# Kernel tuning notes

Hardware: AMD Instinct MI355X
Metric: run time of the kernel (lower is better)

The kernel has to match this reference:

```python
import jax, jax.numpy as jnp
import numpy as np

T, B, L, CTX, H = 512, 512, 16, 64, 128
STATE_DIM, SHOT, PID, DATA = 32, 12, 35, 23


def setup_inputs() -> dict:
    key = jax.random.key(0)
    ks = jax.random.split(key, 64)
    k = iter(ks)
    def rn(shape, s=0.1):
        return (jax.random.normal(next(k), shape) * s).astype(jnp.float32)
    xs = jax.random.normal(next(k), (T, B, DATA), jnp.float32)
    xs = xs.at[:, :, 12].set(jax.random.randint(next(k), (T, B), 0, SHOT).astype(jnp.float32))
    xs = xs.at[:, :, 17].set(jax.random.randint(next(k), (T, B), 0, PID).astype(jnp.float32))
    xs = xs.at[:, :, 20].set(jax.random.randint(next(k), (T, B), 0, SHOT).astype(jnp.float32))
    return dict(
        total_xs=jnp.zeros((1,), jnp.float32),
        xs=xs,
        ts=jnp.linspace(0.0, 2.0, T).astype(jnp.float32),
        noise_std=jnp.asarray(0.1, jnp.float32),
        z0_noise=jax.random.normal(next(k), (B, L), jnp.float32),
        bm_noise=jax.random.normal(next(k), (T - 1, B, L), jnp.float32),
        shot_emb=rn((SHOT, 8)), player_emb=rn((PID, 8)),
        gru_wih=rn((3 * H, STATE_DIM)), gru_whh=rn((3 * H, H)),
        gru_bih=rn((3 * H,)), gru_bhh=rn((3 * H,)),
        enc_w=rn((CTX, H)), enc_b=rn((CTX,)),
        qz0_w=rn((2 * L, CTX)), qz0_b=rn((2 * L,)),
        f_w1=rn((H, L + CTX)), f_b1=rn((H,)), f_w2=rn((H, H)), f_b2=rn((H,)),
        f_w3=rn((L, H)), f_b3=rn((L,)),
        h_w1=rn((H, L)), h_b1=rn((H,)), h_w2=rn((H, H)), h_b2=rn((H,)),
        h_w3=rn((L, H)), h_b3=rn((L,)),
        g_w1=rn((L, H)), g_b1=rn((L, H)), g_w2=rn((L, H)), g_b2=rn((L,)),
        proj_w=rn((STATE_DIM, L)), proj_b=rn((STATE_DIM,)),
        pz0_mean=jnp.zeros((1, L), jnp.float32), pz0_logstd=jnp.zeros((1, L), jnp.float32),
        act_w=rn((128, L)), act_b=rn((128,)),
        act_land_w=rn((2, 128)), act_shot_w=rn((SHOT, 128)), act_move_w=rn((2, 128)),
    )


def _forward(xs, noise_std, shot_emb, player_emb, gru_wih, gru_whh, gru_bih, gru_bhh,
             enc_w, enc_b, qz0_w, qz0_b,
             f_w1, f_b1, f_w2, f_b2, f_w3, f_b3,
             h_w1, h_b1, h_w2, h_b2, h_w3, h_b3,
             g_w1, g_b1, g_w2, g_b2,
             proj_w, proj_b, pz0_mean, pz0_logstd,
             act_w, act_b, act_land_w, act_shot_w, act_move_w,
             ts, z0_noise, bm_noise):
    # --- SDE_embed_and_transform: replace shot/player id cols with embeddings ---
    state = xs[:, :, :18]
    shot_ids = state[:, :, 12].astype(jnp.int32)
    pid_ids = state[:, :, 17].astype(jnp.int32)
    state_t = jnp.concatenate([state[:, :, :12], shot_emb[shot_ids],
                               state[:, :, 13:17], player_emb[pid_ids]], axis=-1)  # (T,B,32)
    xs_t = jnp.concatenate([state_t, xs[:, :, 18:]], axis=-1)  # (T,B,37)
    # --- Encoder: GRU over time-reversed states, linear head, flip back ---
    def gru_step(h, xt):
        gi = xt @ gru_wih.T + gru_bih
        gh = h @ gru_whh.T + gru_bhh
        ir, iz, inn = jnp.split(gi, 3, axis=-1)
        hr, hz, hn = jnp.split(gh, 3, axis=-1)
        r = jax.nn.sigmoid(ir + hr)
        zg = jax.nn.sigmoid(iz + hz)
        n = jnp.tanh(inn + r * hn)
        hnew = (1.0 - zg) * n + zg * h
        return hnew, hnew
    h0 = jnp.zeros((xs.shape[1], gru_whh.shape[1]), xs.dtype)
    _, hs = jax.lax.scan(gru_step, h0, state_t[::-1])
    ctx = (hs @ enc_w.T + enc_b)[::-1]  # (T,B,CTX)
    # --- posterior z0 ---
    qm, qls = jnp.split(ctx[0] @ qz0_w.T + qz0_b, 2, axis=1)
    z0 = qm + jnp.exp(qls) * z0_noise
    # --- Euler-Maruyama with logqp; searchsorted(right) -> ctx[min(i+1,T-1)] = ctx[i+1] ---
    dts = ts[1:] - ts[:-1]  # (T-1,)
    dW = jnp.sqrt(dts)[:, None, None] * bm_noise
    ctx_steps = ctx[1:]
    def mlp3(x, w1, b1, w2, b2, w3, b3):
        h1 = jax.nn.softplus(x @ w1.T + b1)
        h2 = jax.nn.softplus(h1 @ w2.T + b2)
        return h2 @ w3.T + b3
    def g_diag(y):  # (B,L): per-latent-dim scalar nets, batched over L
        hg = jax.nn.softplus(y[:, :, None] * g_w1[None] + g_b1[None])  # (B,L,H)
        return jax.nn.sigmoid(jnp.einsum('blh,lh->bl', hg, g_w2) + g_b2)
    def sde_step(z, inp):
        c, dw, dt = inp
        f_val = mlp3(jnp.concatenate([z, c], axis=1), f_w1, f_b1, f_w2, f_b2, f_w3, f_b3)
        h_val = mlp3(z, h_w1, h_b1, h_w2, h_b2, h_w3, h_b3)
        g_val = g_diag(z)
        u = (f_val - h_val) / g_val
        logr = 0.5 * jnp.sum(u * u, axis=1) * dt
        z_new = z + f_val * dt + g_val * dw
        return z_new, (z_new, logr)
    _, (z_tail, log_ratio) = jax.lax.scan(sde_step, z0, (ctx_steps, dW, dts))
    zs = jnp.concatenate([z0[None], z_tail], axis=0)  # (T,B,L)
    _xs = zs @ proj_w.T + proj_b  # (T,B,32)
    # --- action model losses ---
    a = jax.nn.relu(zs @ act_w.T + act_b)
    land = (a @ act_land_w.T).reshape(-1, 2)
    shot_logits = (a @ act_shot_w.T).reshape(-1, act_shot_w.shape[0])
    move = (a @ act_move_w.T).reshape(-1, 2)
    true_actions = xs_t[:, :, -5:]
    true_land = true_actions[:, :, :2].reshape(-1, 2)
    true_move = true_actions[:, :, 3:].reshape(-1, 2)
    true_shot = true_actions[:, :, 2].astype(jnp.int32).reshape(-1)
    land_loss = jnp.mean((land - true_land) ** 2)
    move_loss = jnp.mean((move - true_move) ** 2)
    logp = jax.nn.log_softmax(shot_logits, axis=-1)
    picked = jnp.take_along_axis(logp, true_shot[:, None], axis=1)[:, 0]
    mask = (true_shot != 0).astype(logp.dtype)  # CrossEntropy ignore_index=0
    shot_loss = -jnp.sum(picked * mask) / jnp.maximum(jnp.sum(mask), 1.0)
    # --- reconstruction log-likelihood ---
    xs_state = xs_t[:, :, :STATE_DIM]
    LOG2PI = 1.8378770664093453
    log_pxs = jnp.mean(jnp.sum(
        -0.5 * ((xs_state - _xs) / noise_std) ** 2 - jnp.log(noise_std) - 0.5 * LOG2PI,
        axis=(0, 2)))
    # --- KL(q(z0) || p(z0)) ---
    var_q = jnp.exp(2.0 * qls)
    var_p = jnp.exp(2.0 * pz0_logstd)
    kl = pz0_logstd - qls + (var_q + (qm - pz0_mean) ** 2) / (2.0 * var_p) - 0.5
    logqp0 = jnp.mean(jnp.sum(kl, axis=1))
    logqp_path = jnp.mean(jnp.sum(log_ratio, axis=0))
    return log_pxs, logqp0 + logqp_path + land_loss + shot_loss + move_loss


def reference(total_xs, xs, ts, noise_std, z0_noise, bm_noise, shot_emb, player_emb,
              gru_wih, gru_whh, gru_bih, gru_bhh, enc_w, enc_b, qz0_w, qz0_b,
              f_w1, f_b1, f_w2, f_b2, f_w3, f_b3, h_w1, h_b1, h_w2, h_b2, h_w3, h_b3,
              g_w1, g_b1, g_w2, g_b2, proj_w, proj_b, pz0_mean, pz0_logstd,
              act_w, act_b, act_land_w, act_shot_w, act_move_w):
    return _forward(xs, noise_std, shot_emb, player_emb, gru_wih, gru_whh, gru_bih, gru_bhh,
                    enc_w, enc_b, qz0_w, qz0_b,
                    f_w1, f_b1, f_w2, f_b2, f_w3, f_b3,
                    h_w1, h_b1, h_w2, h_b2, h_w3, h_b3,
                    g_w1, g_b1, g_w2, g_b2,
                    proj_w, proj_b, pz0_mean, pz0_logstd,
                    act_w, act_b, act_land_w, act_shot_w, act_move_w,
                    ts, z0_noise, bm_noise)
```

## Files before the change

### kernel.cpp

```cpp
#include <hip/hip_runtime.h>
#include <cstdint>

typedef _Float16 f16;
typedef _Float16 f16x2 __attribute__((ext_vector_type(2)));

#define T_STEPS 512
#define B_SZ 512
#define LOG2PI 1.8378770664093453f

__device__ __forceinline__ void barrier_lds() {
  asm volatile("s_waitcnt lgkmcnt(0)" ::: "memory");
  __builtin_amdgcn_s_barrier();
  asm volatile("" ::: "memory");
}

__device__ __forceinline__ uint32_t packh2(float a, float b) {
  f16x2 v; v[0] = (f16)a; v[1] = (f16)b;
  return __builtin_bit_cast(uint32_t, v);
}

__device__ __forceinline__ float fdot2(uint32_t a, uint32_t b, float c) {
#if defined(__AMDGCN__) && __has_builtin(__builtin_amdgcn_fdot2)
  return __builtin_amdgcn_fdot2(__builtin_bit_cast(f16x2, a),
                                __builtin_bit_cast(f16x2, b), c, false);
#else
  f16x2 x = __builtin_bit_cast(f16x2, a), y = __builtin_bit_cast(f16x2, b);
  return c + (float)x[0] * (float)y[0] + (float)x[1] * (float)y[1];
#endif
}

#define DOT4(acc, w0, w1, w2, w3, v)                                     \
  do {                                                                   \
    acc = fdot2((w0), (v).x, acc); acc = fdot2((w1), (v).y, acc);        \
    acc = fdot2((w2), (v).z, acc); acc = fdot2((w3), (v).w, acc);        \
  } while (0)

__device__ __forceinline__ float sigmoidf_(float x) {
  return 1.0f / (1.0f + __expf(-x));
}
__device__ __forceinline__ float tanhf_(float x) {
  float ax = fabsf(x);
  float t = __expf(-2.0f * ax);
  float r = (1.0f - t) / (1.0f + t);
  return copysignf(r, x);
}
__device__ __forceinline__ float softplusf_(float x) {
  return fmaxf(x, 0.0f) + __logf(1.0f + __expf(-fabsf(x)));
}

__global__ __launch_bounds__(256) void k_embed(
    const float* __restrict__ xs, const float* __restrict__ shot_emb,
    const float* __restrict__ player_emb, f16* __restrict__ state_t,
    float* __restrict__ accums) {
  if (blockIdx.x == 0 && threadIdx.x < 16) accums[threadIdx.x] = 0.0f;
  size_t idx = (size_t)blockIdx.x * 256 + threadIdx.x;
  const float* xp = xs + idx * 23;
  f16* op = state_t + idx * 32;
  int sid = (int)xp[12];
  int pid = (int)xp[17];
#pragma unroll
  for (int i = 0; i < 12; ++i) op[i] = (f16)xp[i];
  const float* se = shot_emb + sid * 8;
#pragma unroll
  for (int i = 0; i < 8; ++i) op[12 + i] = (f16)se[i];
#pragma unroll
  for (int i = 0; i < 4; ++i) op[20 + i] = (f16)xp[13 + i];
  const float* pe = player_emb + pid * 8;
#pragma unroll
  for (int i = 0; i < 8; ++i) op[24 + i] = (f16)pe[i];
}

__global__ __launch_bounds__(256) void k_gtab(
    const float* __restrict__ gw1, const float* __restrict__ gb1,
    const float* __restrict__ gw2, const float* __restrict__ gb2,
    float* __restrict__ g_tab) {
  int gid = blockIdx.x * 256 + threadIdx.x;
  int l = gid >> 16, yi = gid & 0xffff;
  f16 hy = __builtin_bit_cast(f16, (unsigned short)yi);
  float y = (float)hy;
  const float* w1 = gw1 + l * 128;
  const float* b1 = gb1 + l * 128;
  const float* w2 = gw2 + l * 128;
  float a0 = 0.f, a1 = 0.f;
#pragma unroll 8
  for (int h = 0; h < 128; h += 2) {
    a0 = fmaf(softplusf_(fmaf(y, w1[h], b1[h])), w2[h], a0);
    a1 = fmaf(softplusf_(fmaf(y, w1[h + 1], b1[h + 1])), w2[h + 1], a1);
  }
  g_tab[gid] = sigmoidf_(a0 + a1 + gb2[l]);
}

__global__ __launch_bounds__(512) void k_gru(
    const f16* __restrict__ state_t, const float* __restrict__ wih,
    const float* __restrict__ whh, const float* __restrict__ bih,
    const float* __restrict__ bhh, const float* __restrict__ enc_w,
    const float* __restrict__ enc_b, const float* __restrict__ qz0_w,
    const float* __restrict__ qz0_b, const float* __restrict__ z0_noise,
    const float* __restrict__ pz0_mean, const float* __restrict__ pz0_logstd,
    f16* __restrict__ ctx, float* __restrict__ z0_out,
    float* __restrict__ accums) {
  __shared__ uint32_t s_x[2][16];
  __shared__ uint32_t s_h[2][64];
  __shared__ float s_gates[2 * 128 * 4];
  __shared__ float s_encp[2 * 64 * 2];
  __shared__ float s_ctx0[2][64];
  __shared__ float s_q[2][32];

  const int tid = threadIdx.x;
  const int bbase = blockIdx.x * 2;
  const uint32_t* stu = (const uint32_t*)state_t;

  uint32_t wA[64];
  uint32_t wB[16];
  float bias0 = 0.f, bias1 = 0.f, encbr = 0.f;

  if (tid < 256) {
    int g = tid >> 7, du = tid & 127;
    const float* whr = whh + (size_t)(g * 128 + du) * 128;
#pragma unroll
    for (int i = 0; i < 64; ++i) wA[i] = packh2(whr[2 * i], whr[2 * i + 1]);
    const float* wxr = wih + (size_t)(g * 128 + du) * 32;
#pragma unroll
    for (int i = 0; i < 16; ++i) wB[i] = packh2(wxr[2 * i], wxr[2 * i + 1]);
    bias0 = bih[g * 128 + du] + bhh[g * 128 + du];
  } else if (tid < 384) {
    int du = tid - 256;
    const float* whr = whh + (size_t)(256 + du) * 128;
#pragma unroll
    for (int i = 0; i < 64; ++i) wA[i] = packh2(whr[2 * i], whr[2 * i + 1]);
    const float* wxr = wih + (size_t)(256 + du) * 32;
#pragma unroll
    for (int i = 0; i < 16; ++i) wB[i] = packh2(wxr[2 * i], wxr[2 * i + 1]);
    bias0 = bih[256 + du];
    bias1 = bhh[256 + du];
  } else {
    int e = tid - 384, c = e & 63, ks = e >> 6;
    const float* wer = enc_w + (size_t)c * 128 + ks * 64;
#pragma unroll
    for (int i = 0; i < 32; ++i) wA[i] = packh2(wer[2 * i], wer[2 * i + 1]);
    encbr = enc_b[c];
  }

  if (tid < 128) s_h[tid >> 6][tid & 63] = 0u;
  if (tid < 32) {
    int b = tid >> 4, i = tid & 15;
    s_x[b][i] = stu[((size_t)(T_STEPS - 1) * B_SZ + bbase + b) * 16 + i];
  }
  float h_old = 0.0f;
  __syncthreads();

  for (int t = T_STEPS - 1; t >= 0; --t) {
    uint4 xpref = make_uint4(0, 0, 0, 0);
    if (tid < 256) {
      int g = tid >> 7, du = tid & 127;
#pragma unroll
      for (int b = 0; b < 2; ++b) {
        float a = bias0;
        const uint4* xq = (const uint4*)&s_x[b][0];
#pragma unroll
        for (int j = 0; j < 4; ++j) {
          uint4 v = xq[j];
          DOT4(a, wB[4 * j], wB[4 * j + 1], wB[4 * j + 2], wB[4 * j + 3], v);
        }
        const uint4* hq = (const uint4*)&s_h[b][0];
#pragma unroll
        for (int j = 0; j < 16; ++j) {
          uint4 v = hq[j];
          DOT4(a, wA[4 * j], wA[4 * j + 1], wA[4 * j + 2], wA[4 * j + 3], v);
        }
        s_gates[(b * 128 + du) * 4 + g] = a;
      }
    } else if (tid < 384) {
      int du = tid - 256;
#pragma unroll
      for (int b = 0; b < 2; ++b) {
        float aI = bias0, aH = bias1;
        const uint4* xq = (const uint4*)&s_x[b][0];
#pragma unroll
        for (int j = 0; j < 4; ++j) {
          uint4 v = xq[j];
          DOT4(aI, wB[4 * j], wB[4 * j + 1], wB[4 * j + 2], wB[4 * j + 3], v);
        }
        const uint4* hq = (const uint4*)&s_h[b][0];
#pragma unroll
        for (int j = 0; j < 16; ++j) {
          uint4 v = hq[j];
          DOT4(aH, wA[4 * j], wA[4 * j + 1], wA[4 * j + 2], wA[4 * j + 3], v);
        }
        s_gates[(b * 128 + du) * 4 + 2] = aI;
        s_gates[(b * 128 + du) * 4 + 3] = aH;
      }
    } else {
      int e = tid - 384, ks = e >> 6, cc = e & 63;
      (void)cc;
      if (t < T_STEPS - 1) {
#pragma unroll
        for (int b = 0; b < 2; ++b) {
          float a = 0.f;
          const uint4* hq = (const uint4*)&s_h[b][ks * 32];
#pragma unroll
          for (int j = 0; j < 8; ++j) {
            uint4 v = hq[j];
            DOT4(a, wA[4 * j], wA[4 * j + 1], wA[4 * j + 2], wA[4 * j + 3], v);
          }
          s_encp[(b * 64 + cc) * 2 + ks] = a;
        }
      }
      if (e < 8 && t > 0) {
        int b = e & 1, q = e >> 1;
        xpref = *(const uint4*)(stu +
                                ((size_t)(t - 1) * B_SZ + bbase + b) * 16 + q * 4);
      }
    }
    barrier_lds();
    if (tid < 256) {
      int b = tid >> 7, du = tid & 127;
      const float4 gt = *(const float4*)&s_gates[(b * 128 + du) * 4];
      float r = sigmoidf_(gt.x), zg = sigmoidf_(gt.y);
      float n = tanhf_(gt.z + r * gt.w);
      float hnew = (1.0f - zg) * n + zg * h_old;
      h_old = hnew;
      ((f16*)&s_h[b][0])[du] = (f16)hnew;
    } else if (tid >= 384) {
      int e = tid - 384, cc = e & 63, b = e >> 6;
      if (t < T_STEPS - 1) {
        float2 p = *(const float2*)&s_encp[(b * 64 + cc) * 2];
        ctx[((size_t)(t + 1) * B_SZ + bbase + b) * 64 + cc] =
            (f16)(p.x + p.y + encbr);
      }
      if (e < 8 && t > 0) {
        int b2 = e & 1, q = e >> 1;
        *(uint4*)&s_x[b2][q * 4] = xpref;
      }
    }
    barrier_lds();
  }

  if (tid >= 384) {
    int e = tid - 384, ks = e >> 6, cc = e & 63;
#pragma unroll
    for (int b = 0; b < 2; ++b) {
      float a = 0.f;
      const uint4* hq = (const uint4*)&s_h[b][ks * 32];
#pragma unroll
      for (int j = 0; j < 8; ++j) {
        uint4 v = hq[j];
        DOT4(a, wA[4 * j], wA[4 * j + 1], wA[4 * j + 2], wA[4 * j + 3], v);
      }
      s_encp[(b * 64 + cc) * 2 + ks] = a;
    }
  }
  __syncthreads();
  if (tid >= 384) {
    int e = tid - 384, cc = e & 63, b = e >> 6;
    float2 p = *(const float2*)&s_encp[(b * 64 + cc) * 2];
    float val = p.x + p.y + encbr;
    ctx[((size_t)bbase + b) * 64 + cc] = (f16)val;
    s_ctx0[b][cc] = val;
  }
  __syncthreads();
  if (tid < 64) {
    int b = tid >> 5, o = tid & 31;
    float acc = qz0_b[o];
#pragma unroll 8
    for (int k = 0; k < 64; ++k) acc += qz0_w[o * 64 + k] * s_ctx0[b][k];
    s_q[b][o] = acc;
  }
  __syncthreads();
  if (tid < 32) {
    int b = tid >> 4, l = tid & 15;
    int bg = bbase + b;
    float qm = s_q[b][l], qls = s_q[b][16 + l];
    float z0v = qm + __expf(qls) * z0_noise[bg * 16 + l];
    z0_out[bg * 16 + l] = z0v;
    float pm = pz0_mean[l], pls = pz0_logstd[l];
    float var_q = __expf(2.0f * qls);
    float var_p = __expf(2.0f * pls);
    float dm = qm - pm;
    float kl = pls - qls + (var_q + dm * dm) / (2.0f * var_p) - 0.5f;
    atomicAdd(&accums[5], kl);
  }
}

__global__ __launch_bounds__(256, 2) void k_sde(
    const f16* __restrict__ ctx, const float* __restrict__ z0_in,
    const float* __restrict__ ts, const float* __restrict__ bm_noise,
    const float* __restrict__ fw1, const float* __restrict__ fb1,
    const float* __restrict__ fw2, const float* __restrict__ fb2,
    const float* __restrict__ fw3, const float* __restrict__ fb3,
    const float* __restrict__ hw1, const float* __restrict__ hb1,
    const float* __restrict__ hw2, const float* __restrict__ hb2,
    const float* __restrict__ hw3, const float* __restrict__ hb3,
    const float* __restrict__ g_tab,
    f16* __restrict__ zs, float* __restrict__ accums) {
  __shared__ uint32_t s_x2[40];
  __shared__ uint32_t s_h1[2][64];
  __shared__ uint32_t s_h2[2][64];
  __shared__ float s_dts[T_STEPS];

  const int tid = threadIdx.x;
  const int bg = blockIdx.x;
  const uint4* ctx4 = (const uint4*)ctx;

  const int r1 = tid >> 1, hh = tid & 1;
  const int mlp2 = tid >> 7, u2 = tid & 127;
  const int l3 = (tid >> 3) & 15;
  const int mlp3 = (tid >> 2) & 1;
  const int kq = tid & 3;
  const bool p3act = (tid < 128);
  const bool zlane = p3act && ((tid & 7) == 0);
  const bool stg = (tid >= 128 && tid < 136);

  uint32_t uw1f[20], uw1h[4], wP2[64], wP3[16];
  float bf1r, bh1r, bias2r, fb3r = 0.f, hb3r = 0.f;
  {
    const float* w = fw1 + (size_t)r1 * 80 + hh * 40;
#pragma unroll
    for (int i = 0; i < 20; ++i) uw1f[i] = packh2(w[2 * i], w[2 * i + 1]);
    bf1r = fb1[r1];
  }
  {
    const float* w = hw1 + (size_t)r1 * 16 + hh * 8;
#pragma unroll
    for (int i = 0; i < 4; ++i) uw1h[i] = packh2(w[2 * i], w[2 * i + 1]);
    bh1r = hb1[r1];
  }
  {
    const float* w = (mlp2 ? hw2 : fw2) + (size_t)u2 * 128;
#pragma unroll
    for (int i = 0; i < 64; ++i) wP2[i] = packh2(w[2 * i], w[2 * i + 1]);
    bias2r = (mlp2 ? hb2 : fb2)[u2];
  }
  if (p3act) {
    const float* w = (mlp3 ? hw3 : fw3) + (size_t)l3 * 128 + kq * 32;
#pragma unroll
    for (int i = 0; i < 16; ++i) wP3[i] = packh2(w[2 * i], w[2 * i + 1]);
    fb3r = fb3[l3];
    hb3r = hb3[l3];
  }
  for (int i = tid; i < T_STEPS - 1; i += 256) s_dts[i] = ts[i + 1] - ts[i];

  float zreg = 0.f, bmc = 0.f, path_acc = 0.f;
  uint4 cpref = make_uint4(0, 0, 0, 0);
  if (zlane) {
    zreg = z0_in[bg * 16 + l3];
    ((f16*)&s_x2[0])[l3] = (f16)zreg;
    zs[(size_t)bg * 16 + l3] = (f16)zreg;
    bmc = bm_noise[(size_t)bg * 16 + l3];
  }
  if (stg) {
    int q = tid - 128;
    uint4 v = ctx4[((size_t)1 * B_SZ + bg) * 8 + q];
    *(uint4*)&s_x2[8 + q * 4] = v;
  }
  __syncthreads();

  for (int t = 0; t < T_STEPS - 1; ++t) {
    float bmn = 0.f, gvp = 0.f;
    if (zlane) {
      unsigned short zb = __builtin_bit_cast(unsigned short, (f16)zreg);
      gvp = g_tab[l3 * 65536 + (int)zb];
      if (t < T_STEPS - 2)
        bmn = bm_noise[((size_t)(t + 1) * B_SZ + bg) * 16 + l3];
    }
    if (stg && t <= T_STEPS - 3)
      cpref = ctx4[((size_t)(t + 2) * B_SZ + bg) * 8 + (tid - 128)];

    {
      const uint4* xq = (const uint4*)&s_x2[0];
      const int base = hh * 5;
      float a0 = 0.f, a1 = 0.f;
      {
        uint4 v0 = xq[base + 0], v1 = xq[base + 1];
        DOT4(a0, uw1f[0], uw1f[1], uw1f[2], uw1f[3], v0);
        DOT4(a1, uw1f[4], uw1f[5], uw1f[6], uw1f[7], v1);
        uint4 v2 = xq[base + 2], v3 = xq[base + 3];
        DOT4(a0, uw1f[8], uw1f[9], uw1f[10], uw1f[11], v2);
        DOT4(a1, uw1f[12], uw1f[13], uw1f[14], uw1f[15], v3);
        uint4 v4 = xq[base + 4];
        DOT4(a0, uw1f[16], uw1f[17], uw1f[18], uw1f[19], v4);
      }
      float af = a0 + a1;
      uint4 vz = xq[hh];
      float ah = 0.f;
      DOT4(ah, uw1h[0], uw1h[1], uw1h[2], uw1h[3], vz);
      float ff = af + __shfl_xor(af, 1);
      float fh = ah + __shfl_xor(ah, 1);
      if (hh == 0)
        ((f16*)&s_h1[0][0])[r1] = (f16)softplusf_(ff + bf1r);
      else
        ((f16*)&s_h1[1][0])[r1] = (f16)softplusf_(fh + bh1r);
    }
    barrier_lds();
    {
      const uint4* hq = (const uint4*)&s_h1[mlp2][0];
      float a0 = 0.f, a1 = 0.f;
#pragma unroll
      for (int j = 0; j < 16; j += 2) {
        uint4 v0 = hq[j], v1 = hq[j + 1];
        DOT4(a0, wP2[4 * j], wP2[4 * j + 1], wP2[4 * j + 2], wP2[4 * j + 3], v0);
        DOT4(a1, wP2[4 * j + 4], wP2[4 * j + 5], wP2[4 * j + 6], wP2[4 * j + 7], v1);
      }
      ((f16*)&s_h2[mlp2][0])[u2] = (f16)softplusf_(a0 + a1 + bias2r);
    }
    barrier_lds();
    if (p3act) {
      const uint4* hq = (const uint4*)&s_h2[mlp3][kq * 16];
      float a0 = 0.f, a1 = 0.f;
#pragma unroll
      for (int j = 0; j < 4; j += 2) {
        uint4 v0 = hq[j], v1 = hq[j + 1];
        DOT4(a0, wP3[4 * j], wP3[4 * j + 1], wP3[4 * j + 2], wP3[4 * j + 3], v0);
        DOT4(a1, wP3[4 * j + 4], wP3[4 * j + 5], wP3[4 * j + 6], wP3[4 * j + 7], v1);
      }
      float a = a0 + a1;
      float s1 = a + __shfl_xor(a, 1);
      float s2 = s1 + __shfl_xor(s1, 2);
      float other = __shfl_xor(s2, 4);
      if ((tid & 7) == 0) {
        float fv = s2 + fb3r;
        float hv = other + hb3r;
        float gv = gvp;
        float dt = s_dts[t];
        float u_ = (fv - hv) / gv;
        float ls = u_ * u_;
        ls += __shfl_xor(ls, 8);
        ls += __shfl_xor(ls, 16);
        ls += __shfl_xor(ls, 32);
        if ((tid & 63) == 0) path_acc += 0.5f * ls * dt;
        float dw = sqrtf(dt) * bmc;
        float zn = zreg + fv * dt + gv * dw;
        zreg = zn;
        ((f16*)&s_x2[0])[l3] = (f16)zn;
        zs[((size_t)(t + 1) * B_SZ + bg) * 16 + l3] = (f16)zn;
        bmc = bmn;
      }
    } else if (stg && t <= T_STEPS - 3) {
      *(uint4*)&s_x2[8 + (tid - 128) * 4] = cpref;
    }
    barrier_lds();
  }
  if (tid == 0 || tid == 64) atomicAdd(&accums[6], path_acc);
}

__global__ __launch_bounds__(256) void k_dec(
    const f16* __restrict__ zs, const f16* __restrict__ state_t,
    const float* __restrict__ xs, const float* __restrict__ proj_w,
    const float* __restrict__ proj_b, const float* __restrict__ act_w,
    const float* __restrict__ act_b, const float* __restrict__ land_w,
    const float* __restrict__ shot_w, const float* __restrict__ move_w,
    float* __restrict__ accums) {
  __shared__ uint32_t s_proj[8 * 32];
  __shared__ uint32_t s_act[8 * 128];
  __shared__ uint32_t s_head[128 * 8];
  __shared__ float s_pb[32], s_ab[128];
  __shared__ float s_red[4 * 5];

  const int tid = threadIdx.x;
  for (int id = tid; id < 8 * 32; id += 256) {
    int kp = id & 7, n = id >> 3;
    s_proj[kp * 32 + n] = packh2(proj_w[n * 16 + 2 * kp], proj_w[n * 16 + 2 * kp + 1]);
  }
  for (int id = tid; id < 8 * 128; id += 256) {
    int kp = id & 7, n = id >> 3;
    s_act[kp * 128 + n] = packh2(act_w[n * 16 + 2 * kp], act_w[n * 16 + 2 * kp + 1]);
  }
  for (int id = tid; id < 128 * 8; id += 256) {
    int j = id >> 3, p = id & 7;
    int h0 = 2 * p, h1 = 2 * p + 1;
    float w0 = (h0 < 2) ? land_w[h0 * 128 + j]
                        : (h0 < 14 ? shot_w[(h0 - 2) * 128 + j]
                                   : move_w[(h0 - 14) * 128 + j]);
    float w1 = (h1 < 2) ? land_w[h1 * 128 + j]
                        : (h1 < 14 ? shot_w[(h1 - 2) * 128 + j]
                                   : move_w[(h1 - 14) * 128 + j]);
    s_head[j * 8 + p] = packh2(w0, w1);
  }
  if (tid < 32) s_pb[tid] = proj_b[tid];
  if (tid < 128) s_ab[tid] = act_b[tid];
  __syncthreads();

  size_t idx = (size_t)blockIdx.x * 256 + tid;
  uint32_t z2[8];
  const uint32_t* zp = (const uint32_t*)(zs + idx * 16);
#pragma unroll
  for (int i = 0; i < 8; ++i) z2[i] = zp[i];
  uint32_t stv[16];
  const uint32_t* stp = (const uint32_t*)(state_t + idx * 32);
#pragma unroll
  for (int i = 0; i < 16; ++i) stv[i] = stp[i];

  float sqsum = 0.0f;
#pragma unroll 4
  for (int i = 0; i < 32; ++i) {
    float acc = s_pb[i];
#pragma unroll
    for (int kp = 0; kp < 8; ++kp) acc = fdot2(s_proj[kp * 32 + i], z2[kp], acc);
    f16x2 sv = __builtin_bit_cast(f16x2, stv[i >> 1]);
    float d = (float)sv[i & 1] - acc;
    sqsum += d * d;
  }

  float hd[16];
#pragma unroll
  for (int i = 0; i < 16; ++i) hd[i] = 0.0f;
#pragma unroll 2
  for (int j = 0; j < 128; ++j) {
    float a = s_ab[j];
#pragma unroll
    for (int kp = 0; kp < 8; ++kp) a = fdot2(s_act[kp * 128 + j], z2[kp], a);
    a = fmaxf(a, 0.0f);
#pragma unroll
    for (int p = 0; p < 8; ++p) {
      f16x2 w = __builtin_bit_cast(f16x2, s_head[j * 8 + p]);
      hd[2 * p] += (float)w[0] * a;
      hd[2 * p + 1] += (float)w[1] * a;
    }
  }
  const float* xp = xs + idx * 23;
  float dl0 = hd[0] - xp[18], dl1 = hd[1] - xp[19];
  float land = dl0 * dl0 + dl1 * dl1;
  float dm0 = hd[14] - xp[21], dm1 = hd[15] - xp[22];
  float move = dm0 * dm0 + dm1 * dm1;
  int sid = (int)xp[20];
  float m = hd[2];
#pragma unroll
  for (int s = 1; s < 12; ++s) m = fmaxf(m, hd[2 + s]);
  float sume = 0.0f;
#pragma unroll
  for (int s = 0; s < 12; ++s) sume += __expf(hd[2 + s] - m);
  float lse = m + __logf(sume);
  float pl = 0.0f;
#pragma unroll
  for (int s = 0; s < 12; ++s)
    if (s == sid) pl = hd[2 + s];
  float picked = 0.0f, cnt = 0.0f;
  if (sid != 0) {
    picked = pl - lse;
    cnt = 1.0f;
  }
  float vals[5] = {sqsum, land, move, picked, cnt};
#pragma unroll
  for (int v = 0; v < 5; ++v) {
    float x = vals[v];
    for (int off = 1; off < 64; off <<= 1) x += __shfl_xor(x, off);
    vals[v] = x;
  }
  int lane = tid & 63, wv = tid >> 6;
  if (lane == 0) {
#pragma unroll
    for (int v = 0; v < 5; ++v) s_red[wv * 5 + v] = vals[v];
  }
  __syncthreads();
  if (tid == 0) {
#pragma unroll
    for (int v = 0; v < 5; ++v) {
      float s = s_red[v] + s_red[5 + v] + s_red[10 + v] + s_red[15 + v];
      atomicAdd(&accums[v], s);
    }
  }
}

__global__ void k_fin(const float* __restrict__ accums,
                      const float* __restrict__ noise_std,
                      float* __restrict__ out) {
  if (threadIdx.x == 0 && blockIdx.x == 0) {
    float sd = noise_std[0];
    float log_pxs = -0.5f * accums[0] / (sd * sd * (float)B_SZ) -
                    (float)T_STEPS * 32.0f * (logf(sd) + 0.5f * LOG2PI);
    float land = accums[1] / (float)(T_STEPS * B_SZ * 2);
    float move = accums[2] / (float)(T_STEPS * B_SZ * 2);
    float shot = -accums[3] / fmaxf(accums[4], 1.0f);
    float out1 = accums[5] / (float)B_SZ + accums[6] / (float)B_SZ + land + shot + move;
    out[0] = log_pxs;
    out[1] = out1;
  }
}

extern "C" void kernel_launch(void* const* d_in, const int* in_sizes, int n_in,
                              void* d_out, int out_size, void* d_ws,
                              size_t ws_size, hipStream_t stream) {
  const float* xs = (const float*)d_in[1];
  const float* ts = (const float*)d_in[2];
  const float* noise_std = (const float*)d_in[3];
  const float* z0_noise = (const float*)d_in[4];
  const float* bm_noise = (const float*)d_in[5];
  const float* shot_emb = (const float*)d_in[6];
  const float* player_emb = (const float*)d_in[7];
  const float* gru_wih = (const float*)d_in[8];
  const float* gru_whh = (const float*)d_in[9];
  const float* gru_bih = (const float*)d_in[10];
  const float* gru_bhh = (const float*)d_in[11];
  const float* enc_w = (const float*)d_in[12];
  const float* enc_b = (const float*)d_in[13];
  const float* qz0_w = (const float*)d_in[14];
  const float* qz0_b = (const float*)d_in[15];
  const float* f_w1 = (const float*)d_in[16];
  const float* f_b1 = (const float*)d_in[17];
  const float* f_w2 = (const float*)d_in[18];
  const float* f_b2 = (const float*)d_in[19];
  const float* f_w3 = (const float*)d_in[20];
  const float* f_b3 = (const float*)d_in[21];
  const float* h_w1 = (const float*)d_in[22];
  const float* h_b1 = (const float*)d_in[23];
  const float* h_w2 = (const float*)d_in[24];
  const float* h_b2 = (const float*)d_in[25];
  const float* h_w3 = (const float*)d_in[26];
  const float* h_b3 = (const float*)d_in[27];
  const float* g_w1 = (const float*)d_in[28];
  const float* g_b1 = (const float*)d_in[29];
  const float* g_w2 = (const float*)d_in[30];
  const float* g_b2 = (const float*)d_in[31];
  const float* proj_w = (const float*)d_in[32];
  const float* proj_b = (const float*)d_in[33];
  const float* pz0_mean = (const float*)d_in[34];
  const float* pz0_logstd = (const float*)d_in[35];
  const float* act_w = (const float*)d_in[36];
  const float* act_b = (const float*)d_in[37];
  const float* act_land_w = (const float*)d_in[38];
  const float* act_shot_w = (const float*)d_in[39];
  const float* act_move_w = (const float*)d_in[40];

  char* ws = (char*)d_ws;
  float* accums = (float*)ws;
  f16* state_t = (f16*)(ws + 256);
  f16* ctx = (f16*)(ws + 256 + 16777216);
  float* z0b = (float*)(ws + 256 + 16777216 + 33554432);
  f16* zs = (f16*)(ws + 256 + 16777216 + 33554432 + 32768);
  float* g_tab = (float*)(ws + 256 + 16777216 + 33554432 + 32768 + 8388608);

  k_embed<<<1024, 256, 0, stream>>>(xs, shot_emb, player_emb, state_t, accums);
  k_gtab<<<4096, 256, 0, stream>>>(g_w1, g_b1, g_w2, g_b2, g_tab);
  k_gru<<<256, 512, 0, stream>>>(state_t, gru_wih, gru_whh, gru_bih, gru_bhh,
                                 enc_w, enc_b, qz0_w, qz0_b, z0_noise, pz0_mean,
                                 pz0_logstd, ctx, z0b, accums);
  k_sde<<<512, 256, 0, stream>>>(ctx, z0b, ts, bm_noise, f_w1, f_b1, f_w2, f_b2,
                                 f_w3, f_b3, h_w1, h_b1, h_w2, h_b2, h_w3, h_b3,
                                 g_tab, zs, accums);
  k_dec<<<1024, 256, 0, stream>>>(zs, state_t, xs, proj_w, proj_b, act_w, act_b,
                                  act_land_w, act_shot_w, act_move_w, accums);
  k_fin<<<1, 64, 0, stream>>>(accums, noise_std, (float*)d_out);
}
```

Baseline: 1.632 ms.

## Restructure GRU kernel to one batch element per 256-thread block

```diff
diff --git a/kernel.cpp b/kernel.cpp
--- a/kernel.cpp
+++ b/kernel.cpp
@@ -90,7 +90,7 @@
   g_tab[gid] = sigmoidf_(a0 + a1 + gb2[l]);
 }
 
-__global__ __launch_bounds__(512) void k_gru(
+__global__ __launch_bounds__(256, 2) void k_gru(
     const f16* __restrict__ state_t, const float* __restrict__ wih,
     const float* __restrict__ whh, const float* __restrict__ bih,
     const float* __restrict__ bhh, const float* __restrict__ enc_w,
@@ -99,181 +99,154 @@
     const float* __restrict__ pz0_mean, const float* __restrict__ pz0_logstd,
     f16* __restrict__ ctx, float* __restrict__ z0_out,
     float* __restrict__ accums) {
-  __shared__ uint32_t s_x[2][16];
-  __shared__ uint32_t s_h[2][64];
-  __shared__ float s_gates[2 * 128 * 4];
-  __shared__ float s_encp[2 * 64 * 2];
-  __shared__ float s_ctx0[2][64];
-  __shared__ float s_q[2][32];
+  __shared__ uint32_t s_x[16];
+  __shared__ uint32_t s_h[64];
+  __shared__ float s_gates[128 * 4];
+  __shared__ float s_encp[64 * 2];
+  __shared__ float s_ctx0[64];
+  __shared__ float s_q[32];
 
   const int tid = threadIdx.x;
-  const int bbase = blockIdx.x * 2;
+  const int bg = blockIdx.x;
+  const int r = tid >> 1, hh = tid & 1;
+  const int ec = r & 63, eks = r >> 6;
   const uint32_t* stu = (const uint32_t*)state_t;
 
-  uint32_t wA[64];
-  uint32_t wB[16];
-  float bias0 = 0.f, bias1 = 0.f, encbr = 0.f;
-
-  if (tid < 256) {
-    int g = tid >> 7, du = tid & 127;
-    const float* whr = whh + (size_t)(g * 128 + du) * 128;
-#pragma unroll
-    for (int i = 0; i < 64; ++i) wA[i] = packh2(whr[2 * i], whr[2 * i + 1]);
-    const float* wxr = wih + (size_t)(g * 128 + du) * 32;
-#pragma unroll
-    for (int i = 0; i < 16; ++i) wB[i] = packh2(wxr[2 * i], wxr[2 * i + 1]);
-    bias0 = bih[g * 128 + du] + bhh[g * 128 + du];
-  } else if (tid < 384) {
-    int du = tid - 256;
-    const float* whr = whh + (size_t)(256 + du) * 128;
-#pragma unroll
-    for (int i = 0; i < 64; ++i) wA[i] = packh2(whr[2 * i], whr[2 * i + 1]);
-    const float* wxr = wih + (size_t)(256 + du) * 32;
-#pragma unroll
-    for (int i = 0; i < 16; ++i) wB[i] = packh2(wxr[2 * i], wxr[2 * i + 1]);
-    bias0 = bih[256 + du];
-    bias1 = bhh[256 + du];
-  } else {
-    int e = tid - 384, c = e & 63, ks = e >> 6;
-    const float* wer = enc_w + (size_t)c * 128 + ks * 64;
-#pragma unroll
-    for (int i = 0; i < 32; ++i) wA[i] = packh2(wer[2 * i], wer[2 * i + 1]);
-    encbr = enc_b[c];
-  }
-
-  if (tid < 128) s_h[tid >> 6][tid & 63] = 0u;
-  if (tid < 32) {
-    int b = tid >> 4, i = tid & 15;
-    s_x[b][i] = stu[((size_t)(T_STEPS - 1) * B_SZ + bbase + b) * 16 + i];
-  }
+  uint32_t wR[32], wZ[32], wN[32];
+  uint32_t wRx[8], wZx[8], wNx[8];
+  uint32_t wE[16];
+  {
+    const float* w0 = whh + (size_t)(0 * 128 + r) * 128 + hh * 64;
+    const float* w1 = whh + (size_t)(1 * 128 + r) * 128 + hh * 64;
+    const float* w2 = whh + (size_t)(2 * 128 + r) * 128 + hh * 64;
+#pragma unroll
+    for (int i = 0; i < 32; ++i) {
+      wR[i] = packh2(w0[2 * i], w0[2 * i + 1]);
+      wZ[i] = packh2(w1[2 * i], w1[2 * i + 1]);
+      wN[i] = packh2(w2[2 * i], w2[2 * i + 1]);
+    }
+    const float* x0 = wih + (size_t)(0 * 128 + r) * 32 + hh * 16;
+    const float* x1 = wih + (size_t)(1 * 128 + r) * 32 + hh * 16;
+    const float* x2 = wih + (size_t)(2 * 128 + r) * 32 + hh * 16;
+#pragma unroll
+    for (int i = 0; i < 8; ++i) {
+      wRx[i] = packh2(x0[2 * i], x0[2 * i + 1]);
+      wZx[i] = packh2(x1[2 * i], x1[2 * i + 1]);
+      wNx[i] = packh2(x2[2 * i], x2[2 * i + 1]);
+    }
+    const float* we = enc_w + (size_t)ec * 128 + eks * 64 + hh * 32;
+#pragma unroll
+    for (int i = 0; i < 16; ++i) wE[i] = packh2(we[2 * i], we[2 * i + 1]);
+  }
+  const float bR = bih[r] + bhh[r];
+  const float bZ = bih[128 + r] + bhh[128 + r];
+  const float bNi = bih[256 + r];
+  const float bNh = bhh[256 + r];
+  float encbr = 0.f;
+  if (tid >= 128 && tid < 192) encbr = enc_b[tid - 128];
+
   float h_old = 0.0f;
+  if (tid < 64) s_h[tid] = 0u;
+  if (tid < 4)
+    *(uint4*)&s_x[tid * 4] =
+        *(const uint4*)(stu + ((size_t)(T_STEPS - 1) * B_SZ + bg) * 16 + tid * 4);
   __syncthreads();
 
   for (int t = T_STEPS - 1; t >= 0; --t) {
     uint4 xpref = make_uint4(0, 0, 0, 0);
-    if (tid < 256) {
-      int g = tid >> 7, du = tid & 127;
-#pragma unroll
-      for (int b = 0; b < 2; ++b) {
-        float a = bias0;
-        const uint4* xq = (const uint4*)&s_x[b][0];
+    if (tid >= 252 && t > 0)
+      xpref = *(const uint4*)(stu +
+                              ((size_t)(t - 1) * B_SZ + bg) * 16 + (tid - 252) * 4);
+    {
+      const uint4* xq = (const uint4*)&s_x[hh * 8];
+      uint4 xv0 = xq[0], xv1 = xq[1];
+      const uint4* hq = (const uint4*)&s_h[hh * 32];
+      float aR = 0.f, aZ = 0.f, aNi = 0.f, aNh = 0.f;
+      DOT4(aR, wRx[0], wRx[1], wRx[2], wRx[3], xv0);
+      DOT4(aR, wRx[4], wRx[5], wRx[6], wRx[7], xv1);
+      DOT4(aZ, wZx[0], wZx[1], wZx[2], wZx[3], xv0);
+      DOT4(aZ, wZx[4], wZx[5], wZx[6], wZx[7], xv1);
+      DOT4(aNi, wNx[0], wNx[1], wNx[2], wNx[3], xv0);
+      DOT4(aNi, wNx[4], wNx[5], wNx[6], wNx[7], xv1);
+#pragma unroll
+      for (int j = 0; j < 8; ++j) {
+        uint4 hv = hq[j];
+        DOT4(aR, wR[4 * j], wR[4 * j + 1], wR[4 * j + 2], wR[4 * j + 3], hv);
+        DOT4(aZ, wZ[4 * j], wZ[4 * j + 1], wZ[4 * j + 2], wZ[4 * j + 3], hv);
+        DOT4(aNh, wN[4 * j], wN[4 * j + 1], wN[4 * j + 2], wN[4 * j + 3], hv);
+      }
+      aR += __shfl_xor(aR, 1);
+      aZ += __shfl_xor(aZ, 1);
+      aNi += __shfl_xor(aNi, 1);
+      aNh += __shfl_xor(aNh, 1);
+      if (hh == 0) {
+        s_gates[r * 4 + 0] = aR + bR;
+        s_gates[r * 4 + 2] = aNi + bNi;
+      } else {
+        s_gates[r * 4 + 1] = aZ + bZ;
+        s_gates[r * 4 + 3] = aNh + bNh;
+      }
+      if (t < T_STEPS - 1) {
+        const uint4* eq = (const uint4*)&s_h[eks * 32 + hh * 16];
+        float aE = 0.f;
 #pragma unroll
         for (int j = 0; j < 4; ++j) {
-          uint4 v = xq[j];
-          DOT4(a, wB[4 * j], wB[4 * j + 1], wB[4 * j + 2], wB[4 * j + 3], v);
+          uint4 ev = eq[j];
+          DOT4(aE, wE[4 * j], wE[4 * j + 1], wE[4 * j + 2], wE[4 * j + 3], ev);
         }
-        const uint4* hq = (const uint4*)&s_h[b][0];
-#pragma unroll
-        for (int j = 0; j < 16; ++j) {
-          uint4 v = hq[j];
-          DOT4(a, wA[4 * j], wA[4 * j + 1], wA[4 * j + 2], wA[4 * j + 3], v);
-        }
-        s_gates[(b * 128 + du) * 4 + g] = a;
-      }
-    } else if (tid < 384) {
-      int du = tid - 256;
-#pragma unroll
-      for (int b = 0; b < 2; ++b) {
-        float aI = bias0, aH = bias1;
-        const uint4* xq = (const uint4*)&s_x[b][0];
-#pragma unroll
-        for (int j = 0; j < 4; ++j) {
-          uint4 v = xq[j];
-          DOT4(aI, wB[4 * j], wB[4 * j + 1], wB[4 * j + 2], wB[4 * j + 3], v);
-        }
-        const uint4* hq = (const uint4*)&s_h[b][0];
-#pragma unroll
-        for (int j = 0; j < 16; ++j) {
-          uint4 v = hq[j];
-          DOT4(aH, wA[4 * j], wA[4 * j + 1], wA[4 * j + 2], wA[4 * j + 3], v);
-        }
-        s_gates[(b * 128 + du) * 4 + 2] = aI;
-        s_gates[(b * 128 + du) * 4 + 3] = aH;
-      }
-    } else {
-      int e = tid - 384, ks = e >> 6, cc = e & 63;
-      (void)cc;
-      if (t < T_STEPS - 1) {
-#pragma unroll
-        for (int b = 0; b < 2; ++b) {
-          float a = 0.f;
-          const uint4* hq = (const uint4*)&s_h[b][ks * 32];
-#pragma unroll
-          for (int j = 0; j < 8; ++j) {
-            uint4 v = hq[j];
-            DOT4(a, wA[4 * j], wA[4 * j + 1], wA[4 * j + 2], wA[4 * j + 3], v);
-          }
-          s_encp[(b * 64 + cc) * 2 + ks] = a;
-        }
-      }
-      if (e < 8 && t > 0) {
-        int b = e & 1, q = e >> 1;
-        xpref = *(const uint4*)(stu +
-                                ((size_t)(t - 1) * B_SZ + bbase + b) * 16 + q * 4);
+        aE += __shfl_xor(aE, 1);
+        if (hh == 0) s_encp[ec * 2 + eks] = aE;
       }
     }
     barrier_lds();
-    if (tid < 256) {
-      int b = tid >> 7, du = tid & 127;
-      const float4 gt = *(const float4*)&s_gates[(b * 128 + du) * 4];
-      float r = sigmoidf_(gt.x), zg = sigmoidf_(gt.y);
-      float n = tanhf_(gt.z + r * gt.w);
+    if (tid < 128) {
+      const float4 gt = *(const float4*)&s_gates[tid * 4];
+      float rr = sigmoidf_(gt.x), zg = sigmoidf_(gt.y);
+      float n = tanhf_(gt.z + rr * gt.w);
       float hnew = (1.0f - zg) * n + zg * h_old;
       h_old = hnew;
-      ((f16*)&s_h[b][0])[du] = (f16)hnew;
-    } else if (tid >= 384) {
-      int e = tid - 384, cc = e & 63, b = e >> 6;
+      ((f16*)&s_h[0])[tid] = (f16)hnew;
+    } else if (tid < 192) {
+      int c = tid - 128;
       if (t < T_STEPS - 1) {
-        float2 p = *(const float2*)&s_encp[(b * 64 + cc) * 2];
-        ctx[((size_t)(t + 1) * B_SZ + bbase + b) * 64 + cc] =
-            (f16)(p.x + p.y + encbr);
-      }
-      if (e < 8 && t > 0) {
-        int b2 = e & 1, q = e >> 1;
-        *(uint4*)&s_x[b2][q * 4] = xpref;
-      }
-    }
+        float v = s_encp[c * 2] + s_encp[c * 2 + 1] + encbr;
+        ctx[((size_t)(t + 1) * B_SZ + bg) * 64 + c] = (f16)v;
+      }
+    }
+    if (tid >= 252 && t > 0) *(uint4*)&s_x[(tid - 252) * 4] = xpref;
     barrier_lds();
   }
 
-  if (tid >= 384) {
-    int e = tid - 384, ks = e >> 6, cc = e & 63;
-#pragma unroll
-    for (int b = 0; b < 2; ++b) {
-      float a = 0.f;
-      const uint4* hq = (const uint4*)&s_h[b][ks * 32];
-#pragma unroll
-      for (int j = 0; j < 8; ++j) {
-        uint4 v = hq[j];
-        DOT4(a, wA[4 * j], wA[4 * j + 1], wA[4 * j + 2], wA[4 * j + 3], v);
-      }
-      s_encp[(b * 64 + cc) * 2 + ks] = a;
-    }
-  }
-  __syncthreads();
-  if (tid >= 384) {
-    int e = tid - 384, cc = e & 63, b = e >> 6;
-    float2 p = *(const float2*)&s_encp[(b * 64 + cc) * 2];
-    float val = p.x + p.y + encbr;
-    ctx[((size_t)bbase + b) * 64 + cc] = (f16)val;
-    s_ctx0[b][cc] = val;
+  {
+    const uint4* eq = (const uint4*)&s_h[eks * 32 + hh * 16];
+    float aE = 0.f;
+#pragma unroll
+    for (int j = 0; j < 4; ++j) {
+      uint4 ev = eq[j];
+      DOT4(aE, wE[4 * j], wE[4 * j + 1], wE[4 * j + 2], wE[4 * j + 3], ev);
+    }
+    aE += __shfl_xor(aE, 1);
+    if (hh == 0) s_encp[ec * 2 + eks] = aE;
   }
   __syncthreads();
   if (tid < 64) {
-    int b = tid >> 5, o = tid & 31;
-    float acc = qz0_b[o];
-#pragma unroll 8
-    for (int k = 0; k < 64; ++k) acc += qz0_w[o * 64 + k] * s_ctx0[b][k];
-    s_q[b][o] = acc;
+    float v = s_encp[tid * 2] + s_encp[tid * 2 + 1] + enc_b[tid];
+    ctx[(size_t)bg * 64 + tid] = (f16)v;
+    s_ctx0[tid] = v;
   }
   __syncthreads();
   if (tid < 32) {
-    int b = tid >> 4, l = tid & 15;
-    int bg = bbase + b;
-    float qm = s_q[b][l], qls = s_q[b][16 + l];
-    float z0v = qm + __expf(qls) * z0_noise[bg * 16 + l];
-    z0_out[bg * 16 + l] = z0v;
-    float pm = pz0_mean[l], pls = pz0_logstd[l];
+    float acc = qz0_b[tid];
+#pragma unroll 8
+    for (int k = 0; k < 64; ++k) acc += qz0_w[tid * 64 + k] * s_ctx0[k];
+    s_q[tid] = acc;
+  }
+  __syncthreads();
+  if (tid < 16) {
+    float qm = s_q[tid], qls = s_q[16 + tid];
+    float z0v = qm + __expf(qls) * z0_noise[bg * 16 + tid];
+    z0_out[bg * 16 + tid] = z0v;
+    float pm = pz0_mean[tid], pls = pz0_logstd[tid];
     float var_q = __expf(2.0f * qls);
     float var_p = __expf(2.0f * pls);
     float dm = qm - pm;
@@ -631,7 +604,7 @@
 
   k_embed<<<1024, 256, 0, stream>>>(xs, shot_emb, player_emb, state_t, accums);
   k_gtab<<<4096, 256, 0, stream>>>(g_w1, g_b1, g_w2, g_b2, g_tab);
-  k_gru<<<256, 512, 0, stream>>>(state_t, gru_wih, gru_whh, gru_bih, gru_bhh,
+  k_gru<<<512, 256, 0, stream>>>(state_t, gru_wih, gru_whh, gru_bih, gru_bhh,
                                  enc_w, enc_b, qz0_w, qz0_b, z0_noise, pz0_mean,
                                  pz0_logstd, ctx, z0b, accums);
   k_sde<<<512, 256, 0, stream>>>(ctx, z0b, ts, bm_noise, f_w1, f_b1, f_w2, f_b2,
```

After: 1.628 ms. No clear change (-0.3%).
